# Kernel tuning notes

Hardware: AMD Instinct MI355X
Metric: run time of the kernel (lower is better)

The kernel has to match this reference:

```python
import jax, jax.numpy as jnp
import numpy as np
import math

V, B, S, D, H, DH, DMEM = 32000, 4, 1024, 1024, 16, 64, 16
HD = H * DH  # == D (required by ff: Linear(n_head*d_head, d_model))
SCALE = 1.0 / math.sqrt(DH)


def pos_table(max_len, d):
    pos = jnp.arange(max_len, dtype=jnp.float32)[:, None]
    freqs = jnp.power(10000.0, -jnp.arange(0, d, 2, dtype=jnp.float32) / d)
    tab = jnp.zeros((max_len, d), dtype=jnp.float32)
    tab = tab.at[:, 0::2].set(jnp.sin(pos * freqs))
    tab = tab.at[:, 1::2].set(jnp.cos(pos * freqs))
    return tab


def layer_norm(x, g, b, eps=1e-5):
    mu = x.mean(-1, keepdims=True)
    var = ((x - mu) ** 2).mean(-1, keepdims=True)
    return (x - mu) * jax.lax.rsqrt(var + eps) * g + b


def mha(h, c, qw, kvw, ow, g, b):
    # h: [B,Sq,D] queries; c: [B,Skv,D] key/value source (post-lnorm, no mask, eval mode)
    q = (h @ qw).reshape(h.shape[0], h.shape[1], H, DH)
    k, v = jnp.split(c @ kvw, 2, axis=-1)
    k = k.reshape(c.shape[0], c.shape[1], H, DH)
    v = v.reshape(c.shape[0], c.shape[1], H, DH)
    scores = jnp.einsum('bind,bjnd->bijn', q, k) * SCALE
    probs = jax.nn.softmax(scores, axis=2)  # softmax over key axis j
    vec = jnp.einsum('bijn,bjnd->bind', probs, v).reshape(h.shape[0], h.shape[1], HD)
    return layer_norm(h + vec @ ow, g, b)


def setup_inputs():
    key = jax.random.key(0)
    ks = jax.random.split(key, 16)
    w = lambda k, shape: jax.random.normal(k, shape, dtype=jnp.float32) * 0.02
    ones = lambda: jnp.ones((D,), dtype=jnp.float32)
    zeros = lambda: jnp.zeros((D,), dtype=jnp.float32)
    return {
        'data': jax.random.randint(ks[0], (B, S), 0, V, dtype=jnp.int32),
        'mem': jnp.zeros((B, DMEM, D), dtype=jnp.float32),
        'emb': w(ks[1], (V, D)),
        'a_qw': w(ks[2], (D, HD)), 'a_kvw': w(ks[3], (D, 2 * HD)), 'a_ow': w(ks[4], (HD, D)),
        'a_g': ones(), 'a_b': zeros(),
        'u_qw': w(ks[5], (D, HD)), 'u_kvw': w(ks[6], (D, 2 * HD)), 'u_ow': w(ks[7], (HD, D)),
        'u_g': ones(), 'u_b': zeros(),
        'ffu_w': w(ks[8], (HD, D)), 'lnu_g': ones(), 'lnu_b': zeros(),
        'o_qw': w(ks[9], (D, HD)), 'o_kvw': w(ks[10], (D, 2 * HD)), 'o_ow': w(ks[11], (HD, D)),
        'o_g': ones(), 'o_b': zeros(),
        'ff2_w': w(ks[12], (HD, D)), 'ln1_g': ones(), 'ln1_b': zeros(),
        'ln2_g': ones(), 'ln2_b': zeros(),
    }


def reference(data, mem, emb, a_qw, a_kvw, a_ow, a_g, a_b,
              u_qw, u_kvw, u_ow, u_g, u_b, ffu_w, lnu_g, lnu_b,
              o_qw, o_kvw, o_ow, o_g, o_b, ff2_w, ln1_g, ln1_b, ln2_g, ln2_b):
    pos = pos_table(S, D)[None, :, :]  # [1,S,D]
    # embedding scale + sinusoidal positional encoding (dropout=0 in eval)
    hids = emb[data] * math.sqrt(D) + pos
    # layer self-attention (post-lnorm residual)
    hids = mha(hids, hids, a_qw, a_kvw, a_ow, a_g, a_b)
    # UpdateAttn: queries from hids, kv over [mem; hids]
    u = mha(hids, jnp.concatenate([mem, hids], axis=1), u_qw, u_kvw, u_ow, u_g, u_b)
    u = u + u @ ffu_w          # output += self.ff(output)
    u = layer_norm(u, lnu_g, lnu_b)
    u = u + (u + pos)          # output += pos_emb(output)
    # memory rollover: keep last d_mem positions of [new_mem; hids]
    new_mem = jnp.concatenate([u, hids], axis=1)[:, -DMEM:, :]
    # OutputAttn: hids attend over [new_mem; hids]
    attn_out = mha(hids, jnp.concatenate([new_mem, hids], axis=1), o_qw, o_kvw, o_ow, o_g, o_b)
    out_attn = layer_norm(hids + attn_out, ln1_g, ln1_b)
    output = layer_norm(out_attn @ ff2_w + out_attn, ln2_g, ln2_b)
    return (output, new_mem)
```

## Files before the change

kernel.cpp:

```cpp
#include <hip/hip_runtime.h>
#include <hip/hip_bf16.h>
#include <math.h>

typedef __bf16 bf16;
typedef __bf16 bf16x4 __attribute__((ext_vector_type(4)));
typedef __bf16 bf16x8 __attribute__((ext_vector_type(8)));
typedef float floatx4 __attribute__((ext_vector_type(4)));

#define LOG2E 1.44269504088896340736f
#define AS1 __attribute__((address_space(1)))
#define AS3 __attribute__((address_space(3)))

__device__ __forceinline__ void async_g2l16(const bf16* g, bf16* l) {
  __builtin_amdgcn_global_load_lds((AS1 void*)(void*)g, (AS3 void*)(void*)l, 16, 0, 0);
}

__global__ __launch_bounds__(256) void embed_kernel(const int* __restrict__ data,
                                                    const float* __restrict__ emb,
                                                    bf16* __restrict__ out) {
  int row = blockIdx.x;
  int s = row & 1023;
  int tok = data[row];
  int d = threadIdx.x * 4;
  floatx4 ev = *(const floatx4*)(emb + (size_t)tok * 1024 + d);
  bf16x4 ov;
#pragma unroll
  for (int pr = 0; pr < 2; pr++) {
    int di = d + pr * 2;
    float e = -(float)di * (13.287712379549449f / 1024.0f);
    float freq = exp2f(e);
    float ang = (float)s * freq;
    float sv, cv;
    __sincosf(ang, &sv, &cv);
    ov[pr * 2] = (bf16)(ev[pr * 2] * 32.0f + sv);
    ov[pr * 2 + 1] = (bf16)(ev[pr * 2 + 1] * 32.0f + cv);
  }
  *(bf16x4*)(out + (size_t)row * 1024 + d) = ov;
}

struct TransArgs {
  const float* src[7];
  bf16* dst[7];
  int cblk[7];
};
__global__ __launch_bounds__(256) void transpose_all_kernel(TransArgs a) {
  int z = blockIdx.z;
  if ((int)blockIdx.x >= a.cblk[z]) return;
  const float* __restrict__ src = a.src[z];
  bf16* __restrict__ dst = a.dst[z];
  int C = a.cblk[z] * 64;
  __shared__ __align__(16) bf16 tile[64][72];
  int c0 = blockIdx.x * 64, r0 = blockIdx.y * 64;
  int t = threadIdx.x;
  int r = t >> 2, cg = (t & 3) * 16;
  const float* sp = src + (size_t)(r0 + r) * C + c0 + cg;
  floatx4 f0 = *(const floatx4*)sp;
  floatx4 f1 = *(const floatx4*)(sp + 4);
  floatx4 f2 = *(const floatx4*)(sp + 8);
  floatx4 f3 = *(const floatx4*)(sp + 12);
  bf16x8 v0, v1;
#pragma unroll
  for (int i = 0; i < 4; i++) {
    v0[i] = (bf16)f0[i];
    v0[4 + i] = (bf16)f1[i];
    v1[i] = (bf16)f2[i];
    v1[4 + i] = (bf16)f3[i];
  }
  *(bf16x8*)&tile[r][cg] = v0;
  *(bf16x8*)&tile[r][cg + 8] = v1;
  __syncthreads();
  bf16x8 o0, o1;
#pragma unroll
  for (int i = 0; i < 8; i++) o0[i] = tile[cg + i][r];
#pragma unroll
  for (int i = 0; i < 8; i++) o1[i] = tile[cg + 8 + i][r];
  bf16* dp = dst + (size_t)(c0 + r) * 1024 + r0 + cg;
  *(bf16x8*)dp = o0;
  *(bf16x8*)(dp + 8) = o1;
}

template <int EPI, int MT>
__global__ __launch_bounds__(256, 3) void gemm_kernel(const bf16* __restrict__ A,
                                                      const bf16* __restrict__ Bt,
                                                      bf16* __restrict__ C0,
                                                      bf16* __restrict__ C1,
                                                      bf16* __restrict__ Vt, int N) {
  constexpr int NJ = (MT == 128) ? 4 : 2;
  constexpr int PA = MT / 32;
  __shared__ __align__(16) bf16 As[MT * 64];
  __shared__ __align__(16) bf16 Bs[128 * 64];
  const int K = 1024;
  int m0 = blockIdx.x * MT, n0 = blockIdx.y * 128;
  int t = threadIdx.x;
  int l = t & 63, w = t >> 6;
  int lr = l & 15, qd = l >> 4;
  int xorb = lr & 7;
  int wrow = __builtin_amdgcn_readfirstlane(t & 192);
  int wm = (MT == 128) ? (w & 1) : 0;
  int wn = (MT == 128) ? (w >> 1) : w;
  int mwbase = wm * 64;
  int nwbase = (MT == 128) ? (wn * 64) : (wn * 32);
  floatx4 acc[4][NJ] = {};
  for (int k0 = 0; k0 < K; k0 += 64) {
#pragma unroll
    for (int p = 0; p < PA; p++) {
      int jl = p * 256 + t;
      int r = jl >> 3;
      int bi = (jl & 7) ^ (r & 7);
      async_g2l16(A + (size_t)(m0 + r) * K + k0 + bi * 8, &As[(p * 256 + wrow) * 8]);
    }
#pragma unroll
    for (int p = 0; p < 4; p++) {
      int jl = p * 256 + t;
      int r = jl >> 3;
      int bi = (jl & 7) ^ (r & 7);
      async_g2l16(Bt + (size_t)(n0 + r) * K + k0 + bi * 8, &Bs[(p * 256 + wrow) * 8]);
    }
    __syncthreads();
#pragma unroll
    for (int c = 0; c < 2; c++) {
      bf16x8 fa[4], fb[NJ];
#pragma unroll
      for (int i = 0; i < 4; i++)
        fa[i] = *(const bf16x8*)&As[(mwbase + i * 16 + lr) * 64 + ((c * 4 + qd) ^ xorb) * 8];
#pragma unroll
      for (int j = 0; j < NJ; j++)
        fb[j] = *(const bf16x8*)&Bs[(nwbase + j * 16 + lr) * 64 + ((c * 4 + qd) ^ xorb) * 8];
#pragma unroll
      for (int i = 0; i < 4; i++)
#pragma unroll
        for (int j = 0; j < NJ; j++)
          acc[i][j] = __builtin_amdgcn_mfma_f32_16x16x32_bf16(fa[i], fb[j], acc[i][j], 0, 0, 0);
    }
    __syncthreads();
  }
#pragma unroll
  for (int i = 0; i < 4; i++) {
    int mbase = m0 + mwbase + i * 16 + qd * 4;
#pragma unroll
    for (int j = 0; j < NJ; j++) {
      int n = n0 + nwbase + j * 16 + lr;
      if (EPI == 0) {
#pragma unroll
        for (int r = 0; r < 4; r++)
          C0[(size_t)(mbase + r) * N + n] = (bf16)acc[i][j][r];
      } else {
        if (n < 1024) {
#pragma unroll
          for (int r = 0; r < 4; r++)
            C0[(size_t)(mbase + r) * 1024 + n] = (bf16)acc[i][j][r];
        } else if (n < 2048) {
#pragma unroll
          for (int r = 0; r < 4; r++)
            C1[(size_t)(mbase + r) * 1024 + (n - 1024)] = (bf16)acc[i][j][r];
        } else {
          int nn = n - 2048;
          int h = nn >> 6, d = nn & 63;
          int bb = mbase >> 10, s = mbase & 1023;
          bf16x4 v = {(bf16)acc[i][j][0], (bf16)acc[i][j][1],
                      (bf16)acc[i][j][2], (bf16)acc[i][j][3]};
          *(bf16x4*)(Vt + ((size_t)((bb * 16 + h) * 64 + d) << 10) + s) = v;
        }
      }
    }
  }
}

__global__ __launch_bounds__(256, 4) void attn_kernel(const bf16* __restrict__ Q,
                                                      const bf16* __restrict__ Kb,
                                                      const bf16* __restrict__ Vt,
                                                      bf16* __restrict__ O,
                                                      int Skv, int memmode) {
  __shared__ __align__(16) bf16 Kt[2][64 * 64];
  __shared__ __align__(16) bf16 Vs[2][64 * 64];
  __shared__ __align__(16) bf16 Ps[4 * 16 * 64];
  int bid = blockIdx.x;
  int qb = bid & 15, h = (bid >> 4) & 15, b = bid >> 8;
  int t = threadIdx.x, w = t >> 6, l = t & 63;
  int lr = l & 15, qd = l >> 4;
  int xorb = lr & 7;
  int wrow = __builtin_amdgcn_readfirstlane(t & 192);
  int pw = w << 10;
  int q0 = qb * 64 + w * 16;
  const bf16* Qrow = Q + (size_t)(b * 1024 + q0 + lr) * 1024 + h * 64;
  bf16x8 aq0 = *(const bf16x8*)(Qrow + qd * 8);
  bf16x8 aq1 = *(const bf16x8*)(Qrow + 32 + qd * 8);
  floatx4 Oacc[4] = {};
  float lsum[4] = {0.f, 0.f, 0.f, 0.f};
  const bf16* Kbase = Kb + (size_t)b * 1024 * 1024 + h * 64;
  const bf16* Vbase = Vt + (size_t)(b * 16 + h) * 64 * 1024;
  int nkt = (Skv + 63) >> 6;

  auto stage = [&](int kt, int bufi) {
    int j0 = kt * 64;
#pragma unroll
    for (int p = 0; p < 2; p++) {
      int jl = p * 256 + t;
      int kr = jl >> 3;
      int bi = (jl & 7) ^ (kr & 7);
      int key = j0 + kr;
      int kc = min(key, Skv - 1);
      int tok = memmode ? (kc < 16 ? 1008 + kc : kc - 16) : kc;
      async_g2l16(Kbase + (size_t)tok * 1024 + bi * 8, &Kt[bufi][(p * 256 + wrow) * 8]);
    }
#pragma unroll
    for (int p = 0; p < 2; p++) {
      int jl = p * 256 + t;
      int dr = jl >> 3;
      int bi = (jl & 7) ^ (dr & 7);
      int jb = j0 + bi * 8;
      int jbc = min(jb, Skv - 8);
      int tok = memmode ? (jbc < 16 ? 1008 + jbc : jbc - 16) : jbc;
      async_g2l16(Vbase + (size_t)dr * 1024 + tok, &Vs[bufi][(p * 256 + wrow) * 8]);
    }
  };

  stage(0, 0);
  for (int kt = 0; kt < nkt; kt++) {
    int buf = kt & 1;
    __syncthreads();
    if (kt + 1 < nkt) stage(kt + 1, buf ^ 1);
    int j0 = kt * 64;
    floatx4 sc[4] = {};
#pragma unroll
    for (int g = 0; g < 4; g++) {
      const bf16* kp = &Kt[buf][(g * 16 + lr) * 64];
      bf16x8 kb0 = *(const bf16x8*)(kp + ((qd ^ xorb) * 8));
      bf16x8 kb1 = *(const bf16x8*)(kp + (((4 + qd) ^ xorb) * 8));
      sc[g] = __builtin_amdgcn_mfma_f32_16x16x32_bf16(aq0, kb0, sc[g], 0, 0, 0);
      sc[g] = __builtin_amdgcn_mfma_f32_16x16x32_bf16(aq1, kb1, sc[g], 0, 0, 0);
    }
#pragma unroll
    for (int g = 0; g < 4; g++) {
      int key = j0 + g * 16 + lr;
      float msk = (key < Skv) ? 1.0f : 0.0f;
      int bcol = (g << 1) | (lr >> 3);
      int c7 = lr & 7;
#pragma unroll
      for (int r = 0; r < 4; r++) {
        int prow = qd * 4 + r;
        float p = exp2f(sc[g][r] * (0.125f * LOG2E)) * msk;
        lsum[r] += p;
        Ps[pw + prow * 64 + (((bcol ^ (prow & 7)) << 3) | c7)] = (bf16)p;
      }
    }
#pragma unroll
    for (int c = 0; c < 2; c++) {
      int cb = c * 4 + qd;
      bf16x8 ap = *(const bf16x8*)&Ps[pw + lr * 64 + ((cb ^ (lr & 7)) << 3)];
#pragma unroll
      for (int tt = 0; tt < 4; tt++) {
        const bf16* vp = &Vs[buf][(tt * 16 + lr) * 64];
        bf16x8 vb = *(const bf16x8*)(vp + ((cb ^ xorb) * 8));
        Oacc[tt] = __builtin_amdgcn_mfma_f32_16x16x32_bf16(ap, vb, Oacc[tt], 0, 0, 0);
      }
    }
  }
#pragma unroll
  for (int r = 0; r < 4; r++) {
    float s = lsum[r];
    s += __shfl_xor(s, 1);
    s += __shfl_xor(s, 2);
    s += __shfl_xor(s, 4);
    s += __shfl_xor(s, 8);
    lsum[r] = 1.0f / s;
  }
#pragma unroll
  for (int tt = 0; tt < 4; tt++)
#pragma unroll
    for (int r = 0; r < 4; r++) {
      size_t orow = (size_t)(b * 1024 + q0 + qd * 4 + r) * 1024 + h * 64 + tt * 16 + lr;
      O[orow] = (bf16)(Oacc[tt][r] * lsum[r]);
    }
}

template <typename OutT>
__global__ __launch_bounds__(256) void ln_kernel(const bf16* __restrict__ x,
                                                 const bf16* __restrict__ res,
                                                 const float* __restrict__ g,
                                                 const float* __restrict__ bta,
                                                 OutT* __restrict__ out) {
  __shared__ float red1[4], red2[4];
  int row = blockIdx.x, t = threadIdx.x;
  size_t base = (size_t)row * 1024 + t * 4;
  bf16x4 xv = *(const bf16x4*)(x + base);
  bf16x4 rv = *(const bf16x4*)(res + base);
  float v[4];
  float s = 0.f;
#pragma unroll
  for (int i = 0; i < 4; i++) {
    v[i] = (float)xv[i] + (float)rv[i];
    s += v[i];
  }
#pragma unroll
  for (int m = 32; m; m >>= 1) s += __shfl_xor(s, m);
  if ((t & 63) == 0) red1[t >> 6] = s;
  __syncthreads();
  float mu = (red1[0] + red1[1] + red1[2] + red1[3]) * (1.0f / 1024.0f);
  float sq = 0.f;
#pragma unroll
  for (int i = 0; i < 4; i++) {
    float dd = v[i] - mu;
    sq += dd * dd;
  }
#pragma unroll
  for (int m = 32; m; m >>= 1) sq += __shfl_xor(sq, m);
  if ((t & 63) == 0) red2[t >> 6] = sq;
  __syncthreads();
  float var = (red2[0] + red2[1] + red2[2] + red2[3]) * (1.0f / 1024.0f);
  float rs = rsqrtf(var + 1e-5f);
  floatx4 gv = *(const floatx4*)(g + t * 4);
  floatx4 bv = *(const floatx4*)(bta + t * 4);
  if constexpr (sizeof(OutT) == 2) {
    bf16x4 ov;
#pragma unroll
    for (int i = 0; i < 4; i++)
      ov[i] = (bf16)((v[i] - mu) * rs * gv[i] + bv[i]);
    *(bf16x4*)(out + base) = ov;
  } else {
    floatx4 ov;
#pragma unroll
    for (int i = 0; i < 4; i++)
      ov[i] = (v[i] - mu) * rs * gv[i] + bv[i];
    *(floatx4*)(out + base) = ov;
  }
}

__global__ __launch_bounds__(256) void dualln_kernel(const bf16* __restrict__ x,
                                                     const bf16* __restrict__ hids,
                                                     const float* __restrict__ g1,
                                                     const float* __restrict__ b1,
                                                     const float* __restrict__ g2,
                                                     const float* __restrict__ b2,
                                                     bf16* __restrict__ out,
                                                     float* __restrict__ newmem) {
  __shared__ float ra[4], rb[4], rc[4], rd[4];
  int row = blockIdx.x, t = threadIdx.x;
  size_t base = (size_t)row * 1024 + t * 4;
  bf16x4 xv = *(const bf16x4*)(x + base);
  bf16x4 hv = *(const bf16x4*)(hids + base);
  float hf[4], v[4];
  float s = 0.f;
#pragma unroll
  for (int i = 0; i < 4; i++) {
    hf[i] = (float)hv[i];
    v[i] = (float)xv[i] + hf[i];
    s += v[i];
  }
  int ss = row & 1023;
  if (ss >= 1008) {
    int bb = row >> 10;
    floatx4 mv = {hf[0], hf[1], hf[2], hf[3]};
    *(floatx4*)(newmem + ((size_t)(bb * 16 + ss - 1008) << 10) + t * 4) = mv;
  }
#pragma unroll
  for (int m = 32; m; m >>= 1) s += __shfl_xor(s, m);
  if ((t & 63) == 0) ra[t >> 6] = s;
  __syncthreads();
  float mu = (ra[0] + ra[1] + ra[2] + ra[3]) * (1.0f / 1024.0f);
  float sq = 0.f;
#pragma unroll
  for (int i = 0; i < 4; i++) {
    float dd = v[i] - mu;
    sq += dd * dd;
  }
#pragma unroll
  for (int m = 32; m; m >>= 1) sq += __shfl_xor(sq, m);
  if ((t & 63) == 0) rb[t >> 6] = sq;
  __syncthreads();
  float var = (rb[0] + rb[1] + rb[2] + rb[3]) * (1.0f / 1024.0f);
  float rs = rsqrtf(var + 1e-5f);
  floatx4 g1v = *(const floatx4*)(g1 + t * 4);
  floatx4 b1v = *(const floatx4*)(b1 + t * 4);
  float y[4];
  float s2 = 0.f;
#pragma unroll
  for (int i = 0; i < 4; i++) {
    float a = (v[i] - mu) * rs * g1v[i] + b1v[i];
    y[i] = hf[i] + a;
    s2 += y[i];
  }
#pragma unroll
  for (int m = 32; m; m >>= 1) s2 += __shfl_xor(s2, m);
  if ((t & 63) == 0) rc[t >> 6] = s2;
  __syncthreads();
  float mu2 = (rc[0] + rc[1] + rc[2] + rc[3]) * (1.0f / 1024.0f);
  float sq2 = 0.f;
#pragma unroll
  for (int i = 0; i < 4; i++) {
    float dd = y[i] - mu2;
    sq2 += dd * dd;
  }
#pragma unroll
  for (int m = 32; m; m >>= 1) sq2 += __shfl_xor(sq2, m);
  if ((t & 63) == 0) rd[t >> 6] = sq2;
  __syncthreads();
  float var2 = (rd[0] + rd[1] + rd[2] + rd[3]) * (1.0f / 1024.0f);
  float rs2 = rsqrtf(var2 + 1e-5f);
  floatx4 g2v = *(const floatx4*)(g2 + t * 4);
  floatx4 b2v = *(const floatx4*)(b2 + t * 4);
  bf16x4 ov;
#pragma unroll
  for (int i = 0; i < 4; i++)
    ov[i] = (bf16)((y[i] - mu2) * rs2 * g2v[i] + b2v[i]);
  *(bf16x4*)(out + base) = ov;
}

extern "C" void kernel_launch(void* const* d_in, const int* in_sizes, int n_in,
                              void* d_out, int out_size, void* d_ws, size_t ws_size,
                              hipStream_t stream) {
  const int* data = (const int*)d_in[0];
  const float* emb = (const float*)d_in[2];
  const float* a_qw = (const float*)d_in[3];
  const float* a_kvw = (const float*)d_in[4];
  const float* a_ow = (const float*)d_in[5];
  const float* a_g = (const float*)d_in[6];
  const float* a_b = (const float*)d_in[7];
  const float* o_qw = (const float*)d_in[16];
  const float* o_kvw = (const float*)d_in[17];
  const float* o_ow = (const float*)d_in[18];
  const float* o_g = (const float*)d_in[19];
  const float* o_b = (const float*)d_in[20];
  const float* ff2_w = (const float*)d_in[21];
  const float* ln1_g = (const float*)d_in[22];
  const float* ln1_b = (const float*)d_in[23];
  const float* ln2_g = (const float*)d_in[24];
  const float* ln2_b = (const float*)d_in[25];
  float* out = (float*)d_out;

  char* ws = (char*)d_ws;
  size_t off = 0;
  auto alloc = [&](size_t elems) {
    bf16* p = (bf16*)(ws + off);
    off += elems * 2;
    return p;
  };
  bf16* Wt_s1 = alloc(3072 * 1024);
  bf16* Wt_s2 = alloc(3072 * 1024);
  bf16* Wt_aow = alloc(1024 * 1024);
  bf16* Wt_oow = alloc(1024 * 1024);
  bf16* Wt_ff2 = alloc(1024 * 1024);
  bf16* hids0 = alloc(4096 * 1024);
  bf16* hids = alloc(4096 * 1024);
  bf16* Qb = alloc(4096 * 1024);
  bf16* Kb = alloc(4096 * 1024);
  bf16* Vtb = alloc(4096 * 1024);
  bf16* vecb = alloc(4096 * 1024);
  bf16* projb = Qb;

  dim3 tb(256);
  TransArgs ta;
  ta.src[0] = a_qw;  ta.dst[0] = Wt_s1;               ta.cblk[0] = 16;
  ta.src[1] = a_kvw; ta.dst[1] = Wt_s1 + 1024 * 1024; ta.cblk[1] = 32;
  ta.src[2] = o_qw;  ta.dst[2] = Wt_s2;               ta.cblk[2] = 16;
  ta.src[3] = o_kvw; ta.dst[3] = Wt_s2 + 1024 * 1024; ta.cblk[3] = 32;
  ta.src[4] = a_ow;  ta.dst[4] = Wt_aow;              ta.cblk[4] = 16;
  ta.src[5] = o_ow;  ta.dst[5] = Wt_oow;              ta.cblk[5] = 16;
  ta.src[6] = ff2_w; ta.dst[6] = Wt_ff2;              ta.cblk[6] = 16;
  transpose_all_kernel<<<dim3(32, 16, 7), tb, 0, stream>>>(ta);

  embed_kernel<<<4096, tb, 0, stream>>>(data, emb, hids0);

  gemm_kernel<1, 128><<<dim3(32, 24), tb, 0, stream>>>(hids0, Wt_s1, Qb, Kb, Vtb, 3072);
  attn_kernel<<<1024, tb, 0, stream>>>(Qb, Kb, Vtb, vecb, 1024, 0);
  gemm_kernel<0, 64><<<dim3(64, 8), tb, 0, stream>>>(vecb, Wt_aow, projb, nullptr, nullptr, 1024);
  ln_kernel<bf16><<<4096, tb, 0, stream>>>(projb, hids0, a_g, a_b, hids);

  gemm_kernel<1, 128><<<dim3(32, 24), tb, 0, stream>>>(hids, Wt_s2, Qb, Kb, Vtb, 3072);
  attn_kernel<<<1024, tb, 0, stream>>>(Qb, Kb, Vtb, vecb, 1040, 1);
  gemm_kernel<0, 64><<<dim3(64, 8), tb, 0, stream>>>(vecb, Wt_oow, projb, nullptr, nullptr, 1024);
  dualln_kernel<<<4096, tb, 0, stream>>>(projb, hids, o_g, o_b, ln1_g, ln1_b, hids0,
                                         out + 4194304);

  gemm_kernel<0, 64><<<dim3(64, 8), tb, 0, stream>>>(hids0, Wt_ff2, projb, nullptr, nullptr, 1024);
  ln_kernel<float><<<4096, tb, 0, stream>>>(projb, hids0, ln2_g, ln2_b, out);
}
```

Measured before the change: 455.2 us.

## Restructure attention to split keys across waves, fold softmax scale into Q

The attention kernel drops LDS staging of K/V and the P round-trip through shared memory. Each wave now processes a 16-key slice of every 64-key tile for all 64 queries, loading K and V directly from global memory into registers. It computes S^T so the probabilities feed straight into a 16x16x16 MFMA for P·V, and reduces the partial outputs across waves through LDS at the end. The softmax scale times log2e is folded into the Q projection epilogue. The embedding kernel is also merged into the weight-transpose launch to save one launch. The trade-offs are redundant global K/V loads with no async prefetch, more accumulator registers, and an extra cross-wave reduction.

```diff
diff --git a/kernel.cpp b/kernel.cpp
--- a/kernel.cpp
+++ b/kernel.cpp
@@ -5,53 +5,64 @@
 typedef __bf16 bf16;
 typedef __bf16 bf16x4 __attribute__((ext_vector_type(4)));
 typedef __bf16 bf16x8 __attribute__((ext_vector_type(8)));
+typedef short shortx4 __attribute__((ext_vector_type(4)));
 typedef float floatx4 __attribute__((ext_vector_type(4)));
 
 #define LOG2E 1.44269504088896340736f
+#define QSCALE 0.18033688011112042f
 #define AS1 __attribute__((address_space(1)))
 #define AS3 __attribute__((address_space(3)))
 
 __device__ __forceinline__ void async_g2l16(const bf16* g, bf16* l) {
   __builtin_amdgcn_global_load_lds((AS1 void*)(void*)g, (AS3 void*)(void*)l, 16, 0, 0);
 }
-
-__global__ __launch_bounds__(256) void embed_kernel(const int* __restrict__ data,
-                                                    const float* __restrict__ emb,
-                                                    bf16* __restrict__ out) {
-  int row = blockIdx.x;
-  int s = row & 1023;
-  int tok = data[row];
-  int d = threadIdx.x * 4;
-  floatx4 ev = *(const floatx4*)(emb + (size_t)tok * 1024 + d);
-  bf16x4 ov;
-#pragma unroll
-  for (int pr = 0; pr < 2; pr++) {
-    int di = d + pr * 2;
-    float e = -(float)di * (13.287712379549449f / 1024.0f);
-    float freq = exp2f(e);
-    float ang = (float)s * freq;
-    float sv, cv;
-    __sincosf(ang, &sv, &cv);
-    ov[pr * 2] = (bf16)(ev[pr * 2] * 32.0f + sv);
-    ov[pr * 2 + 1] = (bf16)(ev[pr * 2 + 1] * 32.0f + cv);
-  }
-  *(bf16x4*)(out + (size_t)row * 1024 + d) = ov;
+__device__ __forceinline__ shortx4 as_s4(bf16x4 v) {
+  shortx4 r;
+  __builtin_memcpy(&r, &v, 8);
+  return r;
 }
 
 struct TransArgs {
   const float* src[7];
   bf16* dst[7];
   int cblk[7];
+  const int* data;
+  const float* emb;
+  bf16* eout;
 };
-__global__ __launch_bounds__(256) void transpose_all_kernel(TransArgs a) {
+__global__ __launch_bounds__(256) void prep_kernel(TransArgs a) {
   int z = blockIdx.z;
+  int t = threadIdx.x;
+  if (z == 7) {
+    int idx = blockIdx.y * 32 + blockIdx.x;
+#pragma unroll
+    for (int r8 = 0; r8 < 8; r8++) {
+      int row = idx * 8 + r8;
+      int s = row & 1023;
+      int tok = a.data[row];
+      int d = t * 4;
+      floatx4 ev = *(const floatx4*)(a.emb + (size_t)tok * 1024 + d);
+      bf16x4 ov;
+#pragma unroll
+      for (int pr = 0; pr < 2; pr++) {
+        int di = d + pr * 2;
+        float freq = exp2f(-(float)di * (13.287712379549449f / 1024.0f));
+        float ang = (float)s * freq;
+        float sv, cv;
+        __sincosf(ang, &sv, &cv);
+        ov[pr * 2] = (bf16)(ev[pr * 2] * 32.0f + sv);
+        ov[pr * 2 + 1] = (bf16)(ev[pr * 2 + 1] * 32.0f + cv);
+      }
+      *(bf16x4*)(a.eout + (size_t)row * 1024 + d) = ov;
+    }
+    return;
+  }
   if ((int)blockIdx.x >= a.cblk[z]) return;
   const float* __restrict__ src = a.src[z];
   bf16* __restrict__ dst = a.dst[z];
   int C = a.cblk[z] * 64;
   __shared__ __align__(16) bf16 tile[64][72];
   int c0 = blockIdx.x * 64, r0 = blockIdx.y * 64;
-  int t = threadIdx.x;
   int r = t >> 2, cg = (t & 3) * 16;
   const float* sp = src + (size_t)(r0 + r) * C + c0 + cg;
   floatx4 f0 = *(const floatx4*)sp;
@@ -148,7 +159,7 @@
         if (n < 1024) {
 #pragma unroll
           for (int r = 0; r < 4; r++)
-            C0[(size_t)(mbase + r) * 1024 + n] = (bf16)acc[i][j][r];
+            C0[(size_t)(mbase + r) * 1024 + n] = (bf16)(acc[i][j][r] * QSCALE);
         } else if (n < 2048) {
 #pragma unroll
           for (int r = 0; r < 4; r++)
@@ -166,112 +177,114 @@
   }
 }
 
-__global__ __launch_bounds__(256, 4) void attn_kernel(const bf16* __restrict__ Q,
-                                                      const bf16* __restrict__ Kb,
-                                                      const bf16* __restrict__ Vt,
-                                                      bf16* __restrict__ O,
-                                                      int Skv, int memmode) {
-  __shared__ __align__(16) bf16 Kt[2][64 * 64];
-  __shared__ __align__(16) bf16 Vs[2][64 * 64];
-  __shared__ __align__(16) bf16 Ps[4 * 16 * 64];
+__global__ __launch_bounds__(256) void attn_kernel(const bf16* __restrict__ Q,
+                                                   const bf16* __restrict__ Kb,
+                                                   const bf16* __restrict__ Vt,
+                                                   bf16* __restrict__ O,
+                                                   int Skv, int memmode) {
+  __shared__ __align__(16) float Ored[3][64][68];
+  __shared__ float Lred[3][64];
   int bid = blockIdx.x;
   int qb = bid & 15, h = (bid >> 4) & 15, b = bid >> 8;
   int t = threadIdx.x, w = t >> 6, l = t & 63;
   int lr = l & 15, qd = l >> 4;
-  int xorb = lr & 7;
-  int wrow = __builtin_amdgcn_readfirstlane(t & 192);
-  int pw = w << 10;
-  int q0 = qb * 64 + w * 16;
-  const bf16* Qrow = Q + (size_t)(b * 1024 + q0 + lr) * 1024 + h * 64;
-  bf16x8 aq0 = *(const bf16x8*)(Qrow + qd * 8);
-  bf16x8 aq1 = *(const bf16x8*)(Qrow + 32 + qd * 8);
-  floatx4 Oacc[4] = {};
+  int q0 = qb * 64;
+  bf16x8 aq[4][2];
+#pragma unroll
+  for (int qg = 0; qg < 4; qg++) {
+    const bf16* Qrow = Q + (size_t)(b * 1024 + q0 + qg * 16 + lr) * 1024 + h * 64;
+    aq[qg][0] = *(const bf16x8*)(Qrow + qd * 8);
+    aq[qg][1] = *(const bf16x8*)(Qrow + 32 + qd * 8);
+  }
+  floatx4 Oacc[4][4] = {};
   float lsum[4] = {0.f, 0.f, 0.f, 0.f};
   const bf16* Kbase = Kb + (size_t)b * 1024 * 1024 + h * 64;
   const bf16* Vbase = Vt + (size_t)(b * 16 + h) * 64 * 1024;
   int nkt = (Skv + 63) >> 6;
-
-  auto stage = [&](int kt, int bufi) {
+  for (int kt = 0; kt < nkt; kt++) {
     int j0 = kt * 64;
-#pragma unroll
-    for (int p = 0; p < 2; p++) {
-      int jl = p * 256 + t;
-      int kr = jl >> 3;
-      int bi = (jl & 7) ^ (kr & 7);
-      int key = j0 + kr;
-      int kc = min(key, Skv - 1);
-      int tok = memmode ? (kc < 16 ? 1008 + kc : kc - 16) : kc;
-      async_g2l16(Kbase + (size_t)tok * 1024 + bi * 8, &Kt[bufi][(p * 256 + wrow) * 8]);
-    }
-#pragma unroll
-    for (int p = 0; p < 2; p++) {
-      int jl = p * 256 + t;
-      int dr = jl >> 3;
-      int bi = (jl & 7) ^ (dr & 7);
-      int jb = j0 + bi * 8;
-      int jbc = min(jb, Skv - 8);
-      int tok = memmode ? (jbc < 16 ? 1008 + jbc : jbc - 16) : jbc;
-      async_g2l16(Vbase + (size_t)dr * 1024 + tok, &Vs[bufi][(p * 256 + wrow) * 8]);
-    }
-  };
-
-  stage(0, 0);
-  for (int kt = 0; kt < nkt; kt++) {
-    int buf = kt & 1;
-    __syncthreads();
-    if (kt + 1 < nkt) stage(kt + 1, buf ^ 1);
-    int j0 = kt * 64;
+    int key = j0 + w * 16 + lr;
+    int kc = min(key, Skv - 1);
+    int tok = memmode ? (kc < 16 ? 1008 + kc : kc - 16) : kc;
+    const bf16* kp = Kbase + (size_t)tok * 1024 + qd * 8;
+    bf16x8 ka0 = *(const bf16x8*)kp;
+    bf16x8 ka1 = *(const bf16x8*)(kp + 32);
+    int jb = j0 + w * 16 + qd * 4;
+    int jc = min(jb, Skv - 4);
+    int tv = memmode ? (jc < 16 ? 1008 + jc : jc - 16) : jc;
+    bf16x4 va[4];
+#pragma unroll
+    for (int dd = 0; dd < 4; dd++)
+      va[dd] = *(const bf16x4*)(Vbase + (size_t)(dd * 16 + lr) * 1024 + tv);
     floatx4 sc[4] = {};
 #pragma unroll
-    for (int g = 0; g < 4; g++) {
-      const bf16* kp = &Kt[buf][(g * 16 + lr) * 64];
-      bf16x8 kb0 = *(const bf16x8*)(kp + ((qd ^ xorb) * 8));
-      bf16x8 kb1 = *(const bf16x8*)(kp + (((4 + qd) ^ xorb) * 8));
-      sc[g] = __builtin_amdgcn_mfma_f32_16x16x32_bf16(aq0, kb0, sc[g], 0, 0, 0);
-      sc[g] = __builtin_amdgcn_mfma_f32_16x16x32_bf16(aq1, kb1, sc[g], 0, 0, 0);
-    }
-#pragma unroll
-    for (int g = 0; g < 4; g++) {
-      int key = j0 + g * 16 + lr;
-      float msk = (key < Skv) ? 1.0f : 0.0f;
-      int bcol = (g << 1) | (lr >> 3);
-      int c7 = lr & 7;
+    for (int qg = 0; qg < 4; qg++) {
+      sc[qg] = __builtin_amdgcn_mfma_f32_16x16x32_bf16(ka0, aq[qg][0], sc[qg], 0, 0, 0);
+      sc[qg] = __builtin_amdgcn_mfma_f32_16x16x32_bf16(ka1, aq[qg][1], sc[qg], 0, 0, 0);
+    }
+    shortx4 ps[4];
+#pragma unroll
+    for (int qg = 0; qg < 4; qg++) {
+      bf16x4 pt;
 #pragma unroll
       for (int r = 0; r < 4; r++) {
-        int prow = qd * 4 + r;
-        float p = exp2f(sc[g][r] * (0.125f * LOG2E)) * msk;
-        lsum[r] += p;
-        Ps[pw + prow * 64 + (((bcol ^ (prow & 7)) << 3) | c7)] = (bf16)p;
+        int kkey = j0 + w * 16 + qd * 4 + r;
+        float p = exp2f(sc[qg][r]);
+        p = (kkey < Skv) ? p : 0.0f;
+        lsum[qg] += p;
+        pt[r] = (bf16)p;
       }
-    }
-#pragma unroll
-    for (int c = 0; c < 2; c++) {
-      int cb = c * 4 + qd;
-      bf16x8 ap = *(const bf16x8*)&Ps[pw + lr * 64 + ((cb ^ (lr & 7)) << 3)];
-#pragma unroll
-      for (int tt = 0; tt < 4; tt++) {
-        const bf16* vp = &Vs[buf][(tt * 16 + lr) * 64];
-        bf16x8 vb = *(const bf16x8*)(vp + ((cb ^ xorb) * 8));
-        Oacc[tt] = __builtin_amdgcn_mfma_f32_16x16x32_bf16(ap, vb, Oacc[tt], 0, 0, 0);
+      ps[qg] = as_s4(pt);
+    }
+#pragma unroll
+    for (int dd = 0; dd < 4; dd++) {
+      shortx4 vs = as_s4(va[dd]);
+#pragma unroll
+      for (int qg = 0; qg < 4; qg++)
+        Oacc[dd][qg] =
+            __builtin_amdgcn_mfma_f32_16x16x16bf16_1k(vs, ps[qg], Oacc[dd][qg], 0, 0, 0);
+    }
+  }
+#pragma unroll
+  for (int qg = 0; qg < 4; qg++) {
+    lsum[qg] += __shfl_xor(lsum[qg], 16);
+    lsum[qg] += __shfl_xor(lsum[qg], 32);
+  }
+  if (w > 0) {
+#pragma unroll
+    for (int dd = 0; dd < 4; dd++)
+#pragma unroll
+      for (int qg = 0; qg < 4; qg++)
+        *(floatx4*)&Ored[w - 1][qg * 16 + lr][dd * 16 + qd * 4] = Oacc[dd][qg];
+    if (qd == 0) {
+#pragma unroll
+      for (int qg = 0; qg < 4; qg++) Lred[w - 1][qg * 16 + lr] = lsum[qg];
+    }
+  }
+  __syncthreads();
+  if (w == 0) {
+    float linv[4];
+#pragma unroll
+    for (int qg = 0; qg < 4; qg++) {
+      float s = lsum[qg] + Lred[0][qg * 16 + lr] + Lred[1][qg * 16 + lr] +
+                Lred[2][qg * 16 + lr];
+      linv[qg] = 1.0f / s;
+    }
+#pragma unroll
+    for (int dd = 0; dd < 4; dd++)
+#pragma unroll
+      for (int qg = 0; qg < 4; qg++) {
+        floatx4 o = Oacc[dd][qg];
+#pragma unroll
+        for (int v = 0; v < 3; v++)
+          o += *(const floatx4*)&Ored[v][qg * 16 + lr][dd * 16 + qd * 4];
+        bf16x4 ob;
+#pragma unroll
+        for (int r = 0; r < 4; r++) ob[r] = (bf16)(o[r] * linv[qg]);
+        *(bf16x4*)(O + (size_t)(b * 1024 + q0 + qg * 16 + lr) * 1024 + h * 64 +
+                   dd * 16 + qd * 4) = ob;
       }
-    }
-  }
-#pragma unroll
-  for (int r = 0; r < 4; r++) {
-    float s = lsum[r];
-    s += __shfl_xor(s, 1);
-    s += __shfl_xor(s, 2);
-    s += __shfl_xor(s, 4);
-    s += __shfl_xor(s, 8);
-    lsum[r] = 1.0f / s;
-  }
-#pragma unroll
-  for (int tt = 0; tt < 4; tt++)
-#pragma unroll
-    for (int r = 0; r < 4; r++) {
-      size_t orow = (size_t)(b * 1024 + q0 + qd * 4 + r) * 1024 + h * 64 + tt * 16 + lr;
-      O[orow] = (bf16)(Oacc[tt][r] * lsum[r]);
-    }
+  }
 }
 
 template <typename OutT>
@@ -457,9 +470,10 @@
   ta.src[4] = a_ow;  ta.dst[4] = Wt_aow;              ta.cblk[4] = 16;
   ta.src[5] = o_ow;  ta.dst[5] = Wt_oow;              ta.cblk[5] = 16;
   ta.src[6] = ff2_w; ta.dst[6] = Wt_ff2;              ta.cblk[6] = 16;
-  transpose_all_kernel<<<dim3(32, 16, 7), tb, 0, stream>>>(ta);
-
-  embed_kernel<<<4096, tb, 0, stream>>>(data, emb, hids0);
+  ta.data = data;
+  ta.emb = emb;
+  ta.eout = hids0;
+  prep_kernel<<<dim3(32, 16, 8), tb, 0, stream>>>(ta);
 
   gemm_kernel<1, 128><<<dim3(32, 24), tb, 0, stream>>>(hids0, Wt_s1, Qb, Kb, Vtb, 3072);
   attn_kernel<<<1024, tb, 0, stream>>>(Qb, Kb, Vtb, vecb, 1024, 0);
```

Result: slower. 475.2 us (+4.4%).
